# Optimization experiments

Measured on AMD Instinct MI355X. Metric: run time of the kernel, lower is better.

The kernel has to match this reference:

```python
import jax, jax.numpy as jnp
import numpy as np

D_MODEL = 1024
N_INPUT = 4096
N_PROCESS = 2048
D_ROUTING = 256
TEMPERATURE = 0.5
LN_EPS = 1e-5


def _gelu(x):
    return jax.nn.gelu(x, approximate=False)  # torch F.gelu default (erf)


def setup_inputs() -> dict:
    key = jax.random.key(0)
    ks = jax.random.split(key, 10)
    B, S = 8, 2048
    x = jax.random.normal(ks[0], (B, S, D_MODEL), dtype=jnp.float32)
    # GlobalRouter query_net: Linear(d_model, 2*d_routing) -> GELU -> LayerNorm -> Linear(2*d_routing, d_routing)
    W1 = jax.random.normal(ks[1], (2 * D_ROUTING, D_MODEL), dtype=jnp.float32) * (2.0 / (D_MODEL + 2 * D_ROUTING)) ** 0.5 * 1.414
    b1 = jnp.zeros((2 * D_ROUTING,), dtype=jnp.float32)
    ln_g = jnp.ones((2 * D_ROUTING,), dtype=jnp.float32)
    ln_b = jnp.zeros((2 * D_ROUTING,), dtype=jnp.float32)
    W2 = jax.random.normal(ks[2], (D_ROUTING, 2 * D_ROUTING), dtype=jnp.float32) * (2.0 / (3 * D_ROUTING)) ** 0.5 * 1.414
    b2 = jnp.zeros((D_ROUTING,), dtype=jnp.float32)
    neuron_keys = jax.random.normal(ks[3], (N_INPUT, D_ROUTING), dtype=jnp.float32) / D_ROUTING ** 0.5 * 1.414
    input_patterns = jax.random.normal(ks[4], (N_INPUT, D_MODEL), dtype=jnp.float32) / D_MODEL ** 0.5 * 1.414
    process_weights = jax.random.normal(ks[5], (N_PROCESS, N_INPUT), dtype=jnp.float32) / N_INPUT ** 0.5 * 1.414
    process_outputs = jax.random.normal(ks[6], (N_PROCESS, D_MODEL), dtype=jnp.float32) / D_MODEL ** 0.5 * 1.414
    return {
        'x': x, 'k_input': 2048, 'k_process': 1024,
        'W1': W1, 'b1': b1, 'ln_g': ln_g, 'ln_b': ln_b, 'W2': W2, 'b2': b2,
        'neuron_keys': neuron_keys, 'input_patterns': input_patterns,
        'process_weights': process_weights, 'process_outputs': process_outputs,
    }


def _forward(x, k_input, k_process, W1, b1, ln_g, ln_b, W2, b2,
             neuron_keys, input_patterns, process_weights, process_outputs):
    B, S, d_model = x.shape
    # ---- GlobalRouter ----
    gctx = jnp.max(x, axis=1)                                  # [B, d_model]
    h = _gelu(gctx @ W1.T + b1)                                # [B, 2*d_routing]
    mu = jnp.mean(h, axis=-1, keepdims=True)
    var = jnp.mean((h - mu) ** 2, axis=-1, keepdims=True)
    h = (h - mu) * jax.lax.rsqrt(var + LN_EPS) * ln_g + ln_b
    query = h @ W2.T + b2                                      # [B, d_routing]
    logits = (query @ neuron_keys.T) / D_ROUTING ** 0.5        # [B, n_input]
    probs = jax.nn.softmax(logits / TEMPERATURE, axis=-1)
    _, input_idx = jax.lax.top_k(logits, k_input)              # [B, k_input]
    one_hot = jnp.zeros_like(probs).at[jnp.arange(B)[:, None], input_idx].set(1.0)
    routing_weights = jax.lax.stop_gradient(one_hot - probs) + probs  # STE
    # ---- input neuron stage ----
    input_acts = _gelu(jnp.einsum('bsd,nd->bsn', x, input_patterns))   # [B,S,n_input]
    weighted = input_acts * routing_weights[:, None, :]
    sel_in = jnp.take_along_axis(weighted, input_idx[:, None, :], axis=2)  # [B,S,k_input]
    # gather process weight columns per batch: [B, n_process, k_input]
    W_sel = jnp.transpose(process_weights[:, input_idx], (1, 0, 2))
    process_acts = _gelu(jnp.einsum('bsk,bpk->bsp', sel_in, W_sel))    # [B,S,n_process]
    # ---- process neuron stage ----
    process_scores = jnp.mean(process_acts, axis=1)                    # [B,n_process]
    _, process_idx = jax.lax.top_k(process_scores, k_process)          # [B,k_process]
    sel_proc = jnp.take_along_axis(process_acts, process_idx[:, None, :], axis=2)  # [B,S,k_process]
    out_sel = process_outputs[process_idx]                             # [B,k_process,d_model]
    return jnp.einsum('bsp,bpd->bsd', sel_proc, out_sel)


def reference(x, k_input, k_process, W1, b1, ln_g, ln_b, W2, b2,
              neuron_keys, input_patterns, process_weights, process_outputs):
    return _forward(x, k_input, k_process, W1, b1, ln_g, ln_b, W2, b2,
                    neuron_keys, input_patterns, process_weights, process_outputs)
```

## Files before the change

### kernel.cpp

```cpp
#include <hip/hip_runtime.h>
#include <stdint.h>

#define B_  8
#define S_  2048
#define DM  1024
#define NI  4096
#define NP  2048
#define DR  256
#define H2  512
#define KI  2048
#define KP  1024
#define LDW 40

typedef __attribute__((ext_vector_type(8))) short bf16x8;
typedef __attribute__((ext_vector_type(4))) float f32x4;
typedef unsigned short ushort;
typedef unsigned int uint;

__device__ __forceinline__ float gelu_erf(float v){
    return 0.5f * v * (1.0f + erff(v * 0.7071067811865476f));
}
__device__ __forceinline__ ushort f2b(float f){
    union { float f; uint u; } a; a.f = f;
    uint r = a.u + 0x7fffu + ((a.u >> 16) & 1u);
    return (ushort)(r >> 16);
}
__device__ __forceinline__ float b2f(ushort u){
    union { uint u; float f; } a; a.u = ((uint)u) << 16; return a.f;
}
__device__ __forceinline__ void cvt8(const float* p, uint4& H, uint4& L){
    uint h[4], l[4];
    #pragma unroll
    for(int i = 0; i < 4; i++){
        ushort h0 = f2b(p[2*i]);   float f0 = b2f(h0); ushort l0 = f2b(p[2*i]   - f0);
        ushort h1 = f2b(p[2*i+1]); float f1 = b2f(h1); ushort l1 = f2b(p[2*i+1] - f1);
        h[i] = (uint)h0 | ((uint)h1 << 16);
        l[i] = (uint)l0 | ((uint)l1 << 16);
    }
    H = uint4{h[0],h[1],h[2],h[3]};
    L = uint4{l[0],l[1],l[2],l[3]};
}
__device__ __forceinline__ void gload_lds16(const void* g, void* l){
    __builtin_amdgcn_global_load_lds((const __attribute__((address_space(1))) void*)g,
                                     (__attribute__((address_space(3))) void*)l, 16, 0, 0);
}

__global__ __launch_bounds__(256) void k_gpart_cvt(const float* __restrict__ x,
                                                   float* __restrict__ gpart,
                                                   ushort* __restrict__ xh,
                                                   ushort* __restrict__ xl){
    int b = blockIdx.x >> 5, ch = blockIdx.x & 31;
    size_t row0 = (size_t)b*S_ + (size_t)ch*64;
    const float4* xb = (const float4*)(x + row0*DM);
    int t = threadIdx.x;
    float4 m = float4{-3.402823466e38f, -3.402823466e38f, -3.402823466e38f, -3.402823466e38f};
    for(int r = 0; r < 64; r++){
        float4 v = xb[(size_t)r*(DM/4) + t];
        ushort hx = f2b(v.x), hy = f2b(v.y), hz = f2b(v.z), hw = f2b(v.w);
        uint2 H{ (uint)hx | ((uint)hy << 16), (uint)hz | ((uint)hw << 16) };
        uint2 L{ (uint)f2b(v.x - b2f(hx)) | ((uint)f2b(v.y - b2f(hy)) << 16),
                 (uint)f2b(v.z - b2f(hz)) | ((uint)f2b(v.w - b2f(hw)) << 16) };
        ((uint2*)(xh + (row0 + r)*DM))[t] = H;
        ((uint2*)(xl + (row0 + r)*DM))[t] = L;
        m.x = fmaxf(m.x, v.x); m.y = fmaxf(m.y, v.y);
        m.z = fmaxf(m.z, v.z); m.w = fmaxf(m.w, v.w);
    }
    ((float4*)(gpart + (size_t)(b*32 + ch)*DM))[t] = m;
}

__global__ __launch_bounds__(256) void k_cvt(const float* __restrict__ src,
                                             ushort* __restrict__ hi,
                                             ushort* __restrict__ lo){
    size_t idx = (size_t)blockIdx.x*256 + threadIdx.x;
    float f[8];
    *(float4*)(f)     = ((const float4*)src)[idx*2];
    *(float4*)(f + 4) = ((const float4*)src)[idx*2 + 1];
    uint4 H, L; cvt8(f, H, L);
    ((uint4*)hi)[idx] = H;
    ((uint4*)lo)[idx] = L;
}

__global__ __launch_bounds__(256) void k_cvt1(const float* __restrict__ src,
                                              ushort* __restrict__ dst){
    size_t idx = (size_t)blockIdx.x*256 + threadIdx.x;
    float f[8];
    *(float4*)(f)     = ((const float4*)src)[idx*2];
    *(float4*)(f + 4) = ((const float4*)src)[idx*2 + 1];
    uint o[4];
    #pragma unroll
    for(int i = 0; i < 4; i++)
        o[i] = (uint)f2b(f[2*i]) | ((uint)f2b(f[2*i+1]) << 16);
    ((uint4*)dst)[idx] = uint4{o[0], o[1], o[2], o[3]};
}

__global__ __launch_bounds__(256) void k_h(const float* __restrict__ gpart,
                                           const float* __restrict__ W1,
                                           const float* __restrict__ b1,
                                           float* __restrict__ h){
    __shared__ float g[DM];
    int b = blockIdx.x >> 3, ig = blockIdx.x & 7;
    int t = threadIdx.x;
    for(int d = t; d < DM; d += 256){
        float m = gpart[(size_t)(b*32)*DM + d];
        for(int c = 1; c < 32; c++) m = fmaxf(m, gpart[(size_t)(b*32 + c)*DM + d]);
        g[d] = m;
    }
    __syncthreads();
    int i  = ig*64 + (t >> 2);
    int dq = (t & 3) * 256;
    const float* wr = W1 + (size_t)i*DM + dq;
    const float* gg = g + dq;
    float s = 0.f;
    for(int d = 0; d < 256; d++) s = fmaf(gg[d], wr[d], s);
    s += __shfl_xor(s, 1);
    s += __shfl_xor(s, 2);
    if((t & 3) == 0) h[b*H2 + i] = gelu_erf(s + b1[i]);
}

__global__ __launch_bounds__(256) void k_query(const float* __restrict__ h,
                                               const float* __restrict__ lng,
                                               const float* __restrict__ lnb,
                                               const float* __restrict__ W2,
                                               const float* __restrict__ b2,
                                               float* __restrict__ query){
    __shared__ float hn[H2];
    __shared__ float red[4];
    int b = blockIdx.x >> 2, qg = blockIdx.x & 3;
    int t = threadIdx.x;
    float v0 = h[b*H2 + t], v1 = h[b*H2 + 256 + t];
    float s = v0 + v1;
    for(int o = 32; o > 0; o >>= 1) s += __shfl_down(s, o);
    if((t & 63) == 0) red[t >> 6] = s;
    __syncthreads();
    float mean = (red[0] + red[1] + red[2] + red[3]) * (1.f/H2);
    __syncthreads();
    float d0 = v0 - mean, d1 = v1 - mean;
    float sq = d0*d0 + d1*d1;
    for(int o = 32; o > 0; o >>= 1) sq += __shfl_down(sq, o);
    if((t & 63) == 0) red[t >> 6] = sq;
    __syncthreads();
    float var  = (red[0] + red[1] + red[2] + red[3]) * (1.f/H2);
    float rstd = rsqrtf(var + 1e-5f);
    hn[t]       = d0*rstd*lng[t]       + lnb[t];
    hn[256 + t] = d1*rstd*lng[256 + t] + lnb[256 + t];
    __syncthreads();
    int q  = qg*64 + (t >> 2);
    int iq = (t & 3) * 128;
    const float* wr = W2 + (size_t)q*H2 + iq;
    float acc = 0.f;
    for(int i2 = 0; i2 < 128; i2++) acc = fmaf(hn[iq + i2], wr[i2], acc);
    acc += __shfl_xor(acc, 1);
    acc += __shfl_xor(acc, 2);
    if((t & 3) == 0) query[b*DR + q] = acc + b2[q];
}

__global__ __launch_bounds__(256) void k_logits(const float* __restrict__ query,
                                                const float* __restrict__ nk,
                                                float* __restrict__ logits){
    __shared__ float q[DR];
    int b = blockIdx.x >> 4, ng = blockIdx.x & 15;
    int t = threadIdx.x;
    if(t < DR) q[t] = query[b*DR + t];
    __syncthreads();
    int n = ng*256 + t;
    const float* kr = nk + (size_t)n*DR;
    float s = 0.f;
    for(int i = 0; i < DR; i++) s = fmaf(q[i], kr[i], s);
    logits[b*NI + n] = s * 0.0625f;
}

template<int N_, int KSEL>
__global__ __launch_bounds__(256) void k_topk(const float* __restrict__ vals,
                                              int* __restrict__ idxout){
    __shared__ unsigned u[N_];
    __shared__ int redc[4];
    __shared__ int sc[256];
    int t = threadIdx.x;
    size_t vbase = (size_t)blockIdx.x * N_;
    size_t obase = (size_t)blockIdx.x * KSEL;
    for(int i = t; i < N_; i += 256){
        unsigned bits = __float_as_uint(vals[vbase + i]);
        u[i] = (bits & 0x80000000u) ? ~bits : (bits | 0x80000000u);
    }
    __syncthreads();
    unsigned lo = 0u, hi = 0xFFFFFFFFu;
    while(lo < hi){
        unsigned mid = lo + (unsigned)((((unsigned long long)(hi - lo)) + 1ull) >> 1);
        int c = 0;
        for(int i = t; i < N_; i += 256) c += (u[i] >= mid) ? 1 : 0;
        for(int o = 32; o > 0; o >>= 1) c += __shfl_down(c, o);
        if((t & 63) == 0) redc[t >> 6] = c;
        __syncthreads();
        int tot = redc[0] + redc[1] + redc[2] + redc[3];
        if(tot >= KSEL) lo = mid; else hi = mid - 1;
        __syncthreads();
    }
    unsigned T = lo;
    const int PER = N_ / 256;
    int base = t * PER;
    int lgt = 0, leq = 0;
    for(int j = 0; j < PER; j++){
        unsigned v = u[base + j];
        lgt += (v > T) ? 1 : 0; leq += (v == T) ? 1 : 0;
    }
    sc[t] = (lgt << 16) | leq;
    __syncthreads();
    for(int o = 1; o < 256; o <<= 1){
        int add = (t >= o) ? sc[t - o] : 0;
        __syncthreads();
        sc[t] += add;
        __syncthreads();
    }
    int need = KSEL - (sc[255] >> 16);
    int ex = (t == 0) ? 0 : sc[t - 1];
    int pos = (ex >> 16) + ((ex & 0xffff) < need ? (ex & 0xffff) : need);
    int eq = ex & 0xffff;
    for(int j = 0; j < PER; j++){
        unsigned v = u[base + j];
        if(v > T){ idxout[obase + pos++] = base + j; }
        else if(v == T){ if(eq < need){ idxout[obase + pos++] = base + j; } eq++; }
    }
}

__global__ __launch_bounds__(256) void k_gemm1(const ushort* __restrict__ xh,
                                               const ushort* __restrict__ xl,
                                               const ushort* __restrict__ ph,
                                               const ushort* __restrict__ pl,
                                               const int* __restrict__ iidx,
                                               ushort* __restrict__ selh,
                                               ushort* __restrict__ sell, int b0){
    __shared__ __align__(16) ushort Ah[2][128*32], Al[2][128*32], Bh[2][128*32], Bl[2][128*32];
    __shared__ int rowmap[128];
    int t = threadIdx.x;
    int g = blockIdx.x >> 8, rest = blockIdx.x & 255;
    int b = b0 + g;
    int mb = rest >> 4, nb = rest & 15;
    int m0 = mb*128, n0 = nb*128;
    ushort* selh_g = selh + (size_t)g*S_*KI;
    ushort* sell_g = sell + (size_t)g*S_*KI;
    if(t < 128) rowmap[t] = iidx[(size_t)b*KI + n0 + t];
    __syncthreads();
    int w = t >> 6, l = t & 63;
    int lr = l >> 2, lc = l & 3;
    int r0 = 32*w + lr, r1 = r0 + 16;
    const ushort* pAh0 = xh + ((size_t)b*S_ + m0 + r0)*DM + lc*8;
    const ushort* pAh1 = xh + ((size_t)b*S_ + m0 + r1)*DM + lc*8;
    const ushort* pAl0 = xl + ((size_t)b*S_ + m0 + r0)*DM + lc*8;
    const ushort* pAl1 = xl + ((size_t)b*S_ + m0 + r1)*DM + lc*8;
    const ushort* pBh0 = ph + (size_t)rowmap[r0]*DM + lc*8;
    const ushort* pBh1 = ph + (size_t)rowmap[r1]*DM + lc*8;
    const ushort* pBl0 = pl + (size_t)rowmap[r0]*DM + lc*8;
    const ushort* pBl1 = pl + (size_t)rowmap[r1]*DM + lc*8;
    int d0 = w*1024, d1 = d0 + 512;
    #define STG1(BUF, KO) do{ \
        gload_lds16(pAh0 + (KO), &Ah[BUF][d0]); \
        gload_lds16(pAh1 + (KO), &Ah[BUF][d1]); \
        gload_lds16(pAl0 + (KO), &Al[BUF][d0]); \
        gload_lds16(pAl1 + (KO), &Al[BUF][d1]); \
        gload_lds16(pBh0 + (KO), &Bh[BUF][d0]); \
        gload_lds16(pBh1 + (KO), &Bh[BUF][d1]); \
        gload_lds16(pBl0 + (KO), &Bl[BUF][d0]); \
        gload_lds16(pBl1 + (KO), &Bl[BUF][d1]); \
    }while(0)
    STG1(0, 0);
    int lm = l & 15, q = l >> 4;
    int mbase = (w >> 1)*64, nbase = (w & 1)*64;
    f32x4 acc[4][4];
    #pragma unroll
    for(int i = 0; i < 4; i++)
      #pragma unroll
      for(int j = 0; j < 4; j++) acc[i][j] = f32x4{0.f,0.f,0.f,0.f};
    int cur = 0;
    for(int k0 = 0; k0 < DM; k0 += 32){
        if(k0 + 32 < DM){
            STG1(cur^1, k0 + 32);
            asm volatile("s_waitcnt vmcnt(8)" ::: "memory");
        }else{
            asm volatile("s_waitcnt vmcnt(0)" ::: "memory");
        }
        __builtin_amdgcn_s_barrier();
        asm volatile("" ::: "memory");
        bf16x8 ahf[4], alf[4];
        #pragma unroll
        for(int mt = 0; mt < 4; mt++){
            ahf[mt] = *(const bf16x8*)(&Ah[cur][(mbase + mt*16 + lm)*32 + q*8]);
            alf[mt] = *(const bf16x8*)(&Al[cur][(mbase + mt*16 + lm)*32 + q*8]);
        }
        __builtin_amdgcn_s_setprio(1);
        #pragma unroll
        for(int nt = 0; nt < 4; nt++){
            bf16x8 bhf = *(const bf16x8*)(&Bh[cur][(nbase + nt*16 + lm)*32 + q*8]);
            bf16x8 blf = *(const bf16x8*)(&Bl[cur][(nbase + nt*16 + lm)*32 + q*8]);
            #pragma unroll
            for(int mt = 0; mt < 4; mt++){
                acc[mt][nt] = __builtin_amdgcn_mfma_f32_16x16x32_bf16(ahf[mt], bhf, acc[mt][nt], 0, 0, 0);
                acc[mt][nt] = __builtin_amdgcn_mfma_f32_16x16x32_bf16(ahf[mt], blf, acc[mt][nt], 0, 0, 0);
                acc[mt][nt] = __builtin_amdgcn_mfma_f32_16x16x32_bf16(alf[mt], bhf, acc[mt][nt], 0, 0, 0);
            }
        }
        __builtin_amdgcn_s_setprio(0);
        asm volatile("s_waitcnt lgkmcnt(0)" ::: "memory");
        __builtin_amdgcn_s_barrier();
        asm volatile("" ::: "memory");
        cur ^= 1;
    }
    #undef STG1
    #pragma unroll
    for(int mt = 0; mt < 4; mt++)
      #pragma unroll
      for(int nt = 0; nt < 4; nt++){
        int col = n0 + nbase + nt*16 + lm;
        #pragma unroll
        for(int i = 0; i < 4; i++){
            int row = m0 + mbase + mt*16 + q*4 + i;
            float gv = gelu_erf(acc[mt][nt][i]);
            ushort hbits = f2b(gv);
            selh_g[(size_t)row*KI + col] = hbits;
            sell_g[(size_t)row*KI + col] = f2b(gv - b2f(hbits));
        }
      }
}

__global__ __launch_bounds__(256) void k_gather_wsel(const float* __restrict__ pw,
                                                     const int* __restrict__ iidx,
                                                     ushort* __restrict__ wh,
                                                     ushort* __restrict__ wl,
                                                     float* __restrict__ scores, int b0){
    int g = blockIdx.x >> 8, pc = blockIdx.x & 255;
    int b = b0 + g;
    ushort* wh_g = wh + (size_t)g*NP*KI;
    ushort* wl_g = wl + (size_t)g*NP*KI;
    int t = threadIdx.x;
    if(t < 8) scores[(size_t)b*NP + pc*8 + t] = 0.f;
    int j0 = t*8;
    int k8[8];
    *(int4*)(k8)     = *(const int4*)(iidx + (size_t)b*KI + j0);
    *(int4*)(k8 + 4) = *(const int4*)(iidx + (size_t)b*KI + j0 + 4);
    for(int r2 = 0; r2 < 8; r2++){
        int p = pc*8 + r2;
        const float* row = pw + (size_t)p*NI;
        uint hh[4], ll[4];
        #pragma unroll
        for(int i = 0; i < 4; i++){
            float v0 = row[k8[2*i]], v1 = row[k8[2*i+1]];
            ushort h0 = f2b(v0), h1 = f2b(v1);
            hh[i] = (uint)h0 | ((uint)h1 << 16);
            ll[i] = (uint)f2b(v0 - b2f(h0)) | ((uint)f2b(v1 - b2f(h1)) << 16);
        }
        *(uint4*)(wh_g + (size_t)p*KI + j0) = uint4{hh[0],hh[1],hh[2],hh[3]};
        *(uint4*)(wl_g + (size_t)p*KI + j0) = uint4{ll[0],ll[1],ll[2],ll[3]};
    }
}

__global__ __launch_bounds__(256) void k_gemm2(const ushort* __restrict__ selh,
                                               const ushort* __restrict__ sell,
                                               const ushort* __restrict__ wh,
                                               const ushort* __restrict__ wl,
                                               ushort* __restrict__ acts,
                                               float* __restrict__ scores, int b0){
    __shared__ __align__(16) ushort Ah[2][128*32], Al[2][128*32], Bh[2][128*32], Bl[2][128*32];
    __shared__ float colsum[128];
    int t = threadIdx.x;
    int g = blockIdx.x >> 8, rest = blockIdx.x & 255;
    int b = b0 + g;
    int mb = rest >> 4, nb = rest & 15;
    int m0 = mb*128, n0 = nb*128;
    const ushort* selh_g = selh + (size_t)g*S_*KI;
    const ushort* sell_g = sell + (size_t)g*S_*KI;
    const ushort* wh_g   = wh   + (size_t)g*NP*KI;
    const ushort* wl_g   = wl   + (size_t)g*NP*KI;
    ushort* acts_g = acts + (size_t)g*S_*NP;
    int w = t >> 6, l = t & 63;
    int lr = l >> 2, lc = l & 3;
    int r0 = 32*w + lr, r1 = r0 + 16;
    const ushort* pAh0 = selh_g + (size_t)(m0 + r0)*KI + lc*8;
    const ushort* pAh1 = selh_g + (size_t)(m0 + r1)*KI + lc*8;
    const ushort* pAl0 = sell_g + (size_t)(m0 + r0)*KI + lc*8;
    const ushort* pAl1 = sell_g + (size_t)(m0 + r1)*KI + lc*8;
    const ushort* pBh0 = wh_g + (size_t)(n0 + r0)*KI + lc*8;
    const ushort* pBh1 = wh_g + (size_t)(n0 + r1)*KI + lc*8;
    const ushort* pBl0 = wl_g + (size_t)(n0 + r0)*KI + lc*8;
    const ushort* pBl1 = wl_g + (size_t)(n0 + r1)*KI + lc*8;
    int d0 = w*1024, d1 = d0 + 512;
    #define STG2(BUF, KO) do{ \
        gload_lds16(pAh0 + (KO), &Ah[BUF][d0]); \
        gload_lds16(pAh1 + (KO), &Ah[BUF][d1]); \
        gload_lds16(pAl0 + (KO), &Al[BUF][d0]); \
        gload_lds16(pAl1 + (KO), &Al[BUF][d1]); \
        gload_lds16(pBh0 + (KO), &Bh[BUF][d0]); \
        gload_lds16(pBh1 + (KO), &Bh[BUF][d1]); \
        gload_lds16(pBl0 + (KO), &Bl[BUF][d0]); \
        gload_lds16(pBl1 + (KO), &Bl[BUF][d1]); \
    }while(0)
    STG2(0, 0);
    int lm = l & 15, q = l >> 4;
    int mbase = (w >> 1)*64, nbase = (w & 1)*64;
    f32x4 acc[4][4];
    #pragma unroll
    for(int i = 0; i < 4; i++)
      #pragma unroll
      for(int j = 0; j < 4; j++) acc[i][j] = f32x4{0.f,0.f,0.f,0.f};
    int cur = 0;
    for(int k0 = 0; k0 < KI; k0 += 32){
        if(k0 + 32 < KI){
            STG2(cur^1, k0 + 32);
            asm volatile("s_waitcnt vmcnt(8)" ::: "memory");
        }else{
            asm volatile("s_waitcnt vmcnt(0)" ::: "memory");
        }
        __builtin_amdgcn_s_barrier();
        asm volatile("" ::: "memory");
        bf16x8 ahf[4], alf[4];
        #pragma unroll
        for(int mt = 0; mt < 4; mt++){
            ahf[mt] = *(const bf16x8*)(&Ah[cur][(mbase + mt*16 + lm)*32 + q*8]);
            alf[mt] = *(const bf16x8*)(&Al[cur][(mbase + mt*16 + lm)*32 + q*8]);
        }
        __builtin_amdgcn_s_setprio(1);
        #pragma unroll
        for(int nt = 0; nt < 4; nt++){
            bf16x8 bhf = *(const bf16x8*)(&Bh[cur][(nbase + nt*16 + lm)*32 + q*8]);
            bf16x8 blf = *(const bf16x8*)(&Bl[cur][(nbase + nt*16 + lm)*32 + q*8]);
            #pragma unroll
            for(int mt = 0; mt < 4; mt++){
                acc[mt][nt] = __builtin_amdgcn_mfma_f32_16x16x32_bf16(ahf[mt], bhf, acc[mt][nt], 0, 0, 0);
                acc[mt][nt] = __builtin_amdgcn_mfma_f32_16x16x32_bf16(ahf[mt], blf, acc[mt][nt], 0, 0, 0);
                acc[mt][nt] = __builtin_amdgcn_mfma_f32_16x16x32_bf16(alf[mt], bhf, acc[mt][nt], 0, 0, 0);
            }
        }
        __builtin_amdgcn_s_setprio(0);
        asm volatile("s_waitcnt lgkmcnt(0)" ::: "memory");
        __builtin_amdgcn_s_barrier();
        asm volatile("" ::: "memory");
        cur ^= 1;
    }
    #undef STG2
    if(t < 128) colsum[t] = 0.f;
    __syncthreads();
    #pragma unroll
    for(int mt = 0; mt < 4; mt++)
      #pragma unroll
      for(int nt = 0; nt < 4; nt++){
        int cb = nbase + nt*16 + lm;
        float s4 = 0.f;
        #pragma unroll
        for(int i = 0; i < 4; i++){
            int row = m0 + mbase + mt*16 + q*4 + i;
            float gv = gelu_erf(acc[mt][nt][i]);
            s4 += gv;
            acts_g[(size_t)row*NP + n0 + cb] = f2b(gv);
        }
        atomicAdd(&colsum[cb], s4);
      }
    __syncthreads();
    if(t < 128) atomicAdd(&scores[(size_t)b*NP + n0 + t], colsum[t]);
}

__global__ __launch_bounds__(256) void k_gather_selacts(const ushort* __restrict__ acts,
                                                        const int* __restrict__ pidx,
                                                        ushort* __restrict__ selacts, int b0){
    int g = blockIdx.x >> 6, sc_ = blockIdx.x & 63;
    int b = b0 + g;
    const ushort* acts_g = acts + (size_t)g*S_*NP;
    ushort* selacts_g = selacts + (size_t)g*S_*KP;
    int t = threadIdx.x;
    int j0 = t*4;
    int4 p4 = *(const int4*)(pidx + (size_t)b*KP + j0);
    const ushort* Ab = acts_g    + ((size_t)sc_*32)*NP;
    ushort*       Ob = selacts_g + ((size_t)sc_*32)*KP;
    for(int r2 = 0; r2 < 32; r2++){
        const ushort* Ar = Ab + (size_t)r2*NP;
        ushort o0 = Ar[p4.x], o1 = Ar[p4.y], o2 = Ar[p4.z], o3 = Ar[p4.w];
        uint2 ov{ (uint)o0 | ((uint)o1 << 16), (uint)o2 | ((uint)o3 << 16) };
        *(uint2*)(Ob + (size_t)r2*KP + j0) = ov;
    }
}

__global__ __launch_bounds__(256) void k_gemm3(const ushort* __restrict__ selacts,
                                               const ushort* __restrict__ poutb,
                                               const int* __restrict__ pidx,
                                               float* __restrict__ out, int b0){
    __shared__ __align__(16) ushort As[2][128*32];
    __shared__ __align__(16) ushort Bs[2][128*LDW];
    __shared__ int pix[KP];
    int t = threadIdx.x;
    int g = blockIdx.x >> 7, rest = blockIdx.x & 127;
    int b = b0 + g;
    int mb = rest >> 3, nb = rest & 7;
    int m0 = mb*128, n0 = nb*128;
    const ushort* sel_g = selacts + (size_t)g*S_*KP;
    int w = t >> 6, l = t & 63;
    int lr = l >> 2, lc = l & 3;
    int r0 = 32*w + lr, r1 = r0 + 16;
    const ushort* pA0 = sel_g + (size_t)(m0 + r0)*KP + lc*8;
    const ushort* pA1 = sel_g + (size_t)(m0 + r1)*KP + lc*8;
    int d0 = w*1024, d1 = d0 + 512;
    gload_lds16(pA0, &As[0][d0]);
    gload_lds16(pA1, &As[0][d1]);
    for(int i = t; i < KP; i += 256) pix[i] = pidx[(size_t)b*KP + i];
    __syncthreads();
    int kk = t >> 3, nc = (t & 7)*16;
    uint4 B0, B1;
    {
        const ushort* bg = poutb + (size_t)pix[kk]*DM + n0 + nc;
        B0 = *(const uint4*)(bg); B1 = *(const uint4*)(bg + 8);
    }
    int lm = l & 15, q = l >> 4;
    int mbase = (w >> 1)*64, nbase = (w & 1)*64;
    f32x4 acc[4][4];
    #pragma unroll
    for(int i = 0; i < 4; i++)
      #pragma unroll
      for(int j = 0; j < 4; j++) acc[i][j] = f32x4{0.f,0.f,0.f,0.f};
    for(int k0 = 0; k0 < KP; k0 += 32){
        int cur = (k0 >> 5) & 1;
        {
            const ushort* pb0 = (const ushort*)&B0;
            const ushort* pb1 = (const ushort*)&B1;
            #pragma unroll
            for(int c = 0; c < 8; c++) Bs[cur][(nc + c)*LDW + kk]     = pb0[c];
            #pragma unroll
            for(int c = 0; c < 8; c++) Bs[cur][(nc + 8 + c)*LDW + kk] = pb1[c];
        }
        if(k0 + 32 < KP){
            gload_lds16(pA0 + (k0 + 32), &As[cur^1][d0]);
            gload_lds16(pA1 + (k0 + 32), &As[cur^1][d1]);
            asm volatile("s_waitcnt vmcnt(2)" ::: "memory");
        }else{
            asm volatile("s_waitcnt vmcnt(0)" ::: "memory");
        }
        asm volatile("s_waitcnt lgkmcnt(0)" ::: "memory");
        __builtin_amdgcn_s_barrier();
        asm volatile("" ::: "memory");
        if(k0 + 32 < KP){
            const ushort* bg = poutb + (size_t)pix[k0 + 32 + kk]*DM + n0 + nc;
            B0 = *(const uint4*)(bg); B1 = *(const uint4*)(bg + 8);
        }
        bf16x8 af[4];
        #pragma unroll
        for(int mt = 0; mt < 4; mt++)
            af[mt] = *(const bf16x8*)(&As[cur][(mbase + mt*16 + lm)*32 + q*8]);
        __builtin_amdgcn_s_setprio(1);
        #pragma unroll
        for(int nt = 0; nt < 4; nt++){
            bf16x8 bf = *(const bf16x8*)(&Bs[cur][(nbase + nt*16 + lm)*LDW + q*8]);
            #pragma unroll
            for(int mt = 0; mt < 4; mt++)
                acc[mt][nt] = __builtin_amdgcn_mfma_f32_16x16x32_bf16(af[mt], bf, acc[mt][nt], 0, 0, 0);
        }
        __builtin_amdgcn_s_setprio(0);
        asm volatile("s_waitcnt lgkmcnt(0)" ::: "memory");
        __builtin_amdgcn_s_barrier();
        asm volatile("" ::: "memory");
    }
    float* Cb = out + (size_t)b*S_*DM;
    #pragma unroll
    for(int mt = 0; mt < 4; mt++)
      #pragma unroll
      for(int nt = 0; nt < 4; nt++){
        int col = n0 + nbase + nt*16 + lm;
        #pragma unroll
        for(int i = 0; i < 4; i++){
            int row = m0 + mbase + mt*16 + q*4 + i;
            Cb[(size_t)row*DM + col] = acc[mt][nt][i];
        }
      }
}

extern "C" void kernel_launch(void* const* d_in, const int* in_sizes, int n_in,
                              void* d_out, int out_size, void* d_ws, size_t ws_size,
                              hipStream_t stream){
    const float* x    = (const float*)d_in[0];
    const float* W1   = (const float*)d_in[3];
    const float* b1   = (const float*)d_in[4];
    const float* lng  = (const float*)d_in[5];
    const float* lnb  = (const float*)d_in[6];
    const float* W2   = (const float*)d_in[7];
    const float* b2   = (const float*)d_in[8];
    const float* nk   = (const float*)d_in[9];
    const float* patt = (const float*)d_in[10];
    const float* pw   = (const float*)d_in[11];
    const float* pout = (const float*)d_in[12];
    float* out = (float*)d_out;

    auto al256 = [](size_t v){ return (v + 255) & ~(size_t)255; };
    const size_t fixed =
        al256((size_t)B_*32*DM*4) + al256((size_t)B_*H2*4) + al256((size_t)B_*DR*4) +
        al256((size_t)B_*NI*4)    + al256((size_t)B_*KI*4) + al256((size_t)B_*NP*4) +
        al256((size_t)B_*KP*4) +
        2*al256((size_t)B_*S_*DM*2) + 2*al256((size_t)NI*DM*2) + al256((size_t)NP*DM*2);
    const size_t perb = (size_t)S_*KI*2*2 + (size_t)NP*KI*2*2 + (size_t)S_*NP*2 + (size_t)S_*KP*2 + 6*256;
    int G = 8;
    while(G > 1 && fixed + (size_t)G*perb > ws_size) G >>= 1;
    if(fixed + (size_t)G*perb > ws_size) return;

    char* wsp = (char*)d_ws;
    size_t off = 0;
    auto alloc = [&](size_t bytes) -> void* {
        void* p = wsp + off;
        off += (bytes + 255) & ~(size_t)255;
        return p;
    };
    float*  gpart   = (float*) alloc((size_t)B_*32*DM*4);
    float*  h       = (float*) alloc((size_t)B_*H2*4);
    float*  query   = (float*) alloc((size_t)B_*DR*4);
    float*  logits  = (float*) alloc((size_t)B_*NI*4);
    int*    iidx    = (int*)   alloc((size_t)B_*KI*4);
    float*  scores  = (float*) alloc((size_t)B_*NP*4);
    int*    pidx    = (int*)   alloc((size_t)B_*KP*4);
    ushort* xh      = (ushort*)alloc((size_t)B_*S_*DM*2);
    ushort* xl      = (ushort*)alloc((size_t)B_*S_*DM*2);
    ushort* patth   = (ushort*)alloc((size_t)NI*DM*2);
    ushort* pattl   = (ushort*)alloc((size_t)NI*DM*2);
    ushort* poutb   = (ushort*)alloc((size_t)NP*DM*2);
    ushort* selh    = (ushort*)alloc((size_t)G*S_*KI*2);
    ushort* sell    = (ushort*)alloc((size_t)G*S_*KI*2);
    ushort* wselh   = (ushort*)alloc((size_t)G*NP*KI*2);
    ushort* wsell   = (ushort*)alloc((size_t)G*NP*KI*2);
    ushort* acts    = (ushort*)alloc((size_t)G*S_*NP*2);
    ushort* selacts = (ushort*)alloc((size_t)G*S_*KP*2);

    dim3 blk(256);
    k_gpart_cvt<<<B_*32, blk, 0, stream>>>(x, gpart, xh, xl);
    k_cvt   <<<(NI*DM/8)/256, blk, 0, stream>>>(patt, patth, pattl);
    k_cvt1  <<<(NP*DM/8)/256, blk, 0, stream>>>(pout, poutb);
    k_h     <<<64,  blk, 0, stream>>>(gpart, W1, b1, h);
    k_query <<<32,  blk, 0, stream>>>(h, lng, lnb, W2, b2, query);
    k_logits<<<128, blk, 0, stream>>>(query, nk, logits);
    k_topk<NI, KI><<<B_, blk, 0, stream>>>(logits, iidx);
    for(int b0 = 0; b0 < B_; b0 += G){
        k_gemm1        <<<G*256, blk, 0, stream>>>(xh, xl, patth, pattl, iidx, selh, sell, b0);
        k_gather_wsel  <<<G*256, blk, 0, stream>>>(pw, iidx, wselh, wsell, scores, b0);
        k_gemm2        <<<G*256, blk, 0, stream>>>(selh, sell, wselh, wsell, acts, scores, b0);
        k_topk<NP, KP> <<<G,     blk, 0, stream>>>(scores + (size_t)b0*NP, pidx + (size_t)b0*KP);
        k_gather_selacts<<<G*64, blk, 0, stream>>>(acts, pidx, selacts, b0);
        k_gemm3        <<<G*128, blk, 0, stream>>>(selacts, poutb, pidx, out, b0);
    }
}
```

Measured before the change: 1.297 ms.

## Fuse preprocessing kernels, merge gather into GEMM1 launch, widen topk and logits

```diff
diff --git a/kernel.cpp b/kernel.cpp
--- a/kernel.cpp
+++ b/kernel.cpp
@@ -45,52 +45,53 @@
                                      (__attribute__((address_space(3))) void*)l, 16, 0, 0);
 }
 
-__global__ __launch_bounds__(256) void k_gpart_cvt(const float* __restrict__ x,
-                                                   float* __restrict__ gpart,
-                                                   ushort* __restrict__ xh,
-                                                   ushort* __restrict__ xl){
-    int b = blockIdx.x >> 5, ch = blockIdx.x & 31;
-    size_t row0 = (size_t)b*S_ + (size_t)ch*64;
-    const float4* xb = (const float4*)(x + row0*DM);
-    int t = threadIdx.x;
-    float4 m = float4{-3.402823466e38f, -3.402823466e38f, -3.402823466e38f, -3.402823466e38f};
-    for(int r = 0; r < 64; r++){
-        float4 v = xb[(size_t)r*(DM/4) + t];
-        ushort hx = f2b(v.x), hy = f2b(v.y), hz = f2b(v.z), hw = f2b(v.w);
-        uint2 H{ (uint)hx | ((uint)hy << 16), (uint)hz | ((uint)hw << 16) };
-        uint2 L{ (uint)f2b(v.x - b2f(hx)) | ((uint)f2b(v.y - b2f(hy)) << 16),
-                 (uint)f2b(v.z - b2f(hz)) | ((uint)f2b(v.w - b2f(hw)) << 16) };
-        ((uint2*)(xh + (row0 + r)*DM))[t] = H;
-        ((uint2*)(xl + (row0 + r)*DM))[t] = L;
-        m.x = fmaxf(m.x, v.x); m.y = fmaxf(m.y, v.y);
-        m.z = fmaxf(m.z, v.z); m.w = fmaxf(m.w, v.w);
-    }
-    ((float4*)(gpart + (size_t)(b*32 + ch)*DM))[t] = m;
-}
-
-__global__ __launch_bounds__(256) void k_cvt(const float* __restrict__ src,
-                                             ushort* __restrict__ hi,
-                                             ushort* __restrict__ lo){
-    size_t idx = (size_t)blockIdx.x*256 + threadIdx.x;
-    float f[8];
-    *(float4*)(f)     = ((const float4*)src)[idx*2];
-    *(float4*)(f + 4) = ((const float4*)src)[idx*2 + 1];
-    uint4 H, L; cvt8(f, H, L);
-    ((uint4*)hi)[idx] = H;
-    ((uint4*)lo)[idx] = L;
-}
-
-__global__ __launch_bounds__(256) void k_cvt1(const float* __restrict__ src,
-                                              ushort* __restrict__ dst){
-    size_t idx = (size_t)blockIdx.x*256 + threadIdx.x;
-    float f[8];
-    *(float4*)(f)     = ((const float4*)src)[idx*2];
-    *(float4*)(f + 4) = ((const float4*)src)[idx*2 + 1];
-    uint o[4];
-    #pragma unroll
-    for(int i = 0; i < 4; i++)
-        o[i] = (uint)f2b(f[2*i]) | ((uint)f2b(f[2*i+1]) << 16);
-    ((uint4*)dst)[idx] = uint4{o[0], o[1], o[2], o[3]};
+__global__ __launch_bounds__(256) void k_pre(const float* __restrict__ x,
+                                             const float* __restrict__ patt,
+                                             const float* __restrict__ pout,
+                                             float* __restrict__ gpart,
+                                             ushort* __restrict__ xh,
+                                             ushort* __restrict__ xl,
+                                             ushort* __restrict__ patth,
+                                             ushort* __restrict__ pattl,
+                                             ushort* __restrict__ poutb){
+    int bid = blockIdx.x;
+    int t = threadIdx.x;
+    if(bid < 512){
+        int b = bid >> 6, ch = bid & 63;
+        size_t row0 = (size_t)b*S_ + (size_t)ch*32;
+        const float4* xb = (const float4*)(x + row0*DM);
+        float4 m = float4{-3.402823466e38f, -3.402823466e38f, -3.402823466e38f, -3.402823466e38f};
+        for(int r = 0; r < 32; r++){
+            float4 v = xb[(size_t)r*(DM/4) + t];
+            ushort hx = f2b(v.x), hy = f2b(v.y), hz = f2b(v.z), hw = f2b(v.w);
+            uint2 H{ (uint)hx | ((uint)hy << 16), (uint)hz | ((uint)hw << 16) };
+            uint2 L{ (uint)f2b(v.x - b2f(hx)) | ((uint)f2b(v.y - b2f(hy)) << 16),
+                     (uint)f2b(v.z - b2f(hz)) | ((uint)f2b(v.w - b2f(hw)) << 16) };
+            ((uint2*)(xh + (row0 + r)*DM))[t] = H;
+            ((uint2*)(xl + (row0 + r)*DM))[t] = L;
+            m.x = fmaxf(m.x, v.x); m.y = fmaxf(m.y, v.y);
+            m.z = fmaxf(m.z, v.z); m.w = fmaxf(m.w, v.w);
+        }
+        ((float4*)(gpart + (size_t)(b*64 + ch)*DM))[t] = m;
+    }else if(bid < 2560){
+        size_t idx = (size_t)(bid - 512)*256 + t;
+        float f[8];
+        *(float4*)(f)     = ((const float4*)patt)[idx*2];
+        *(float4*)(f + 4) = ((const float4*)patt)[idx*2 + 1];
+        uint4 H, L; cvt8(f, H, L);
+        ((uint4*)patth)[idx] = H;
+        ((uint4*)pattl)[idx] = L;
+    }else{
+        size_t idx = (size_t)(bid - 2560)*256 + t;
+        float f[8];
+        *(float4*)(f)     = ((const float4*)pout)[idx*2];
+        *(float4*)(f + 4) = ((const float4*)pout)[idx*2 + 1];
+        uint o[4];
+        #pragma unroll
+        for(int i = 0; i < 4; i++)
+            o[i] = (uint)f2b(f[2*i]) | ((uint)f2b(f[2*i+1]) << 16);
+        ((uint4*)poutb)[idx] = uint4{o[0], o[1], o[2], o[3]};
+    }
 }
 
 __global__ __launch_bounds__(256) void k_h(const float* __restrict__ gpart,
@@ -101,8 +102,8 @@
     int b = blockIdx.x >> 3, ig = blockIdx.x & 7;
     int t = threadIdx.x;
     for(int d = t; d < DM; d += 256){
-        float m = gpart[(size_t)(b*32)*DM + d];
-        for(int c = 1; c < 32; c++) m = fmaxf(m, gpart[(size_t)(b*32 + c)*DM + d]);
+        float m = gpart[(size_t)(b*64)*DM + d];
+        for(int c = 1; c < 64; c++) m = fmaxf(m, gpart[(size_t)(b*64 + c)*DM + d]);
         g[d] = m;
     }
     __syncthreads();
@@ -157,28 +158,35 @@
 __global__ __launch_bounds__(256) void k_logits(const float* __restrict__ query,
                                                 const float* __restrict__ nk,
                                                 float* __restrict__ logits){
-    __shared__ float q[DR];
+    __shared__ float4 q4[DR/4];
     int b = blockIdx.x >> 4, ng = blockIdx.x & 15;
     int t = threadIdx.x;
-    if(t < DR) q[t] = query[b*DR + t];
-    __syncthreads();
-    int n = ng*256 + t;
-    const float* kr = nk + (size_t)n*DR;
-    float s = 0.f;
-    for(int i = 0; i < DR; i++) s = fmaf(q[i], kr[i], s);
-    logits[b*NI + n] = s * 0.0625f;
+    if(t < 64) q4[t] = ((const float4*)(query + (size_t)b*DR))[t];
+    __syncthreads();
+    int w = t >> 6, lane = t & 63;
+    float4 qv = q4[lane];
+    int nbase = ng*256 + w*64;
+    #pragma unroll 2
+    for(int i = 0; i < 64; i++){
+        int n = nbase + i;
+        float4 v = ((const float4*)(nk + (size_t)n*DR))[lane];
+        float p = v.x*qv.x + v.y*qv.y + v.z*qv.z + v.w*qv.w;
+        p += __shfl_down(p, 32); p += __shfl_down(p, 16); p += __shfl_down(p, 8);
+        p += __shfl_down(p, 4);  p += __shfl_down(p, 2);  p += __shfl_down(p, 1);
+        if(lane == 0) logits[(size_t)b*NI + n] = p * 0.0625f;
+    }
 }
 
 template<int N_, int KSEL>
-__global__ __launch_bounds__(256) void k_topk(const float* __restrict__ vals,
-                                              int* __restrict__ idxout){
+__global__ __launch_bounds__(1024) void k_topk(const float* __restrict__ vals,
+                                               int* __restrict__ idxout){
     __shared__ unsigned u[N_];
-    __shared__ int redc[4];
-    __shared__ int sc[256];
+    __shared__ int redc[16];
+    __shared__ int sc[1024];
     int t = threadIdx.x;
     size_t vbase = (size_t)blockIdx.x * N_;
     size_t obase = (size_t)blockIdx.x * KSEL;
-    for(int i = t; i < N_; i += 256){
+    for(int i = t; i < N_; i += 1024){
         unsigned bits = __float_as_uint(vals[vbase + i]);
         u[i] = (bits & 0x80000000u) ? ~bits : (bits | 0x80000000u);
     }
@@ -187,16 +195,18 @@
     while(lo < hi){
         unsigned mid = lo + (unsigned)((((unsigned long long)(hi - lo)) + 1ull) >> 1);
         int c = 0;
-        for(int i = t; i < N_; i += 256) c += (u[i] >= mid) ? 1 : 0;
+        for(int i = t; i < N_; i += 1024) c += (u[i] >= mid) ? 1 : 0;
         for(int o = 32; o > 0; o >>= 1) c += __shfl_down(c, o);
         if((t & 63) == 0) redc[t >> 6] = c;
         __syncthreads();
-        int tot = redc[0] + redc[1] + redc[2] + redc[3];
+        int tot = 0;
+        #pragma unroll
+        for(int i = 0; i < 16; i++) tot += redc[i];
         if(tot >= KSEL) lo = mid; else hi = mid - 1;
         __syncthreads();
     }
     unsigned T = lo;
-    const int PER = N_ / 256;
+    const int PER = N_ / 1024;
     int base = t * PER;
     int lgt = 0, leq = 0;
     for(int j = 0; j < PER; j++){
@@ -205,13 +215,13 @@
     }
     sc[t] = (lgt << 16) | leq;
     __syncthreads();
-    for(int o = 1; o < 256; o <<= 1){
+    for(int o = 1; o < 1024; o <<= 1){
         int add = (t >= o) ? sc[t - o] : 0;
         __syncthreads();
         sc[t] += add;
         __syncthreads();
     }
-    int need = KSEL - (sc[255] >> 16);
+    int need = KSEL - (sc[1023] >> 16);
     int ex = (t == 0) ? 0 : sc[t - 1];
     int pos = (ex >> 16) + ((ex & 0xffff) < need ? (ex & 0xffff) : need);
     int eq = ex & 0xffff;
@@ -222,18 +232,62 @@
     }
 }
 
-__global__ __launch_bounds__(256) void k_gemm1(const ushort* __restrict__ xh,
-                                               const ushort* __restrict__ xl,
-                                               const ushort* __restrict__ ph,
-                                               const ushort* __restrict__ pl,
-                                               const int* __restrict__ iidx,
-                                               ushort* __restrict__ selh,
-                                               ushort* __restrict__ sell, int b0){
-    __shared__ __align__(16) ushort Ah[2][128*32], Al[2][128*32], Bh[2][128*32], Bl[2][128*32];
-    __shared__ int rowmap[128];
-    int t = threadIdx.x;
-    int g = blockIdx.x >> 8, rest = blockIdx.x & 255;
+__global__ __launch_bounds__(256) void k_stage1(const ushort* __restrict__ xh,
+                                                const ushort* __restrict__ xl,
+                                                const ushort* __restrict__ ph,
+                                                const ushort* __restrict__ pl,
+                                                const float* __restrict__ pw,
+                                                const int* __restrict__ iidx,
+                                                ushort* __restrict__ selh,
+                                                ushort* __restrict__ sell,
+                                                ushort* __restrict__ wh,
+                                                ushort* __restrict__ wl,
+                                                float* __restrict__ scores, int b0){
+    __shared__ __align__(16) ushort sm[33024];
+    int t = threadIdx.x;
+    int role = blockIdx.x & 1;
+    int id   = blockIdx.x >> 1;
+    int g = id >> 8;
     int b = b0 + g;
+    if(role == 1){
+        float* row = (float*)sm;
+        int pc = id & 255;
+        ushort* wh_g = wh + (size_t)g*NP*KI;
+        ushort* wl_g = wl + (size_t)g*NP*KI;
+        if(t < 8) scores[(size_t)b*NP + pc*8 + t] = 0.f;
+        int j0 = t*8;
+        int k8[8];
+        *(int4*)(k8)     = *(const int4*)(iidx + (size_t)b*KI + j0);
+        *(int4*)(k8 + 4) = *(const int4*)(iidx + (size_t)b*KI + j0 + 4);
+        for(int r2 = 0; r2 < 8; r2++){
+            int p = pc*8 + r2;
+            const float4* src = (const float4*)(pw + (size_t)p*NI);
+            float4 rv0 = src[t], rv1 = src[t + 256], rv2 = src[t + 512], rv3 = src[t + 768];
+            __syncthreads();
+            ((float4*)row)[t]       = rv0;
+            ((float4*)row)[t + 256] = rv1;
+            ((float4*)row)[t + 512] = rv2;
+            ((float4*)row)[t + 768] = rv3;
+            __syncthreads();
+            uint hh[4], ll[4];
+            #pragma unroll
+            for(int i = 0; i < 4; i++){
+                float v0 = row[k8[2*i]], v1 = row[k8[2*i+1]];
+                ushort h0 = f2b(v0), h1 = f2b(v1);
+                hh[i] = (uint)h0 | ((uint)h1 << 16);
+                ll[i] = (uint)f2b(v0 - b2f(h0)) | ((uint)f2b(v1 - b2f(h1)) << 16);
+            }
+            *(uint4*)(wh_g + (size_t)p*KI + j0) = uint4{hh[0],hh[1],hh[2],hh[3]};
+            *(uint4*)(wl_g + (size_t)p*KI + j0) = uint4{ll[0],ll[1],ll[2],ll[3]};
+        }
+        return;
+    }
+    ushort* Ah = sm;
+    ushort* Al = sm + 8192;
+    ushort* Bh = sm + 16384;
+    ushort* Bl = sm + 24576;
+    int* rowmap = (int*)(sm + 32768);
+    int rest = id & 255;
     int mb = rest >> 4, nb = rest & 15;
     int m0 = mb*128, n0 = nb*128;
     ushort* selh_g = selh + (size_t)g*S_*KI;
@@ -253,14 +307,14 @@
     const ushort* pBl1 = pl + (size_t)rowmap[r1]*DM + lc*8;
     int d0 = w*1024, d1 = d0 + 512;
     #define STG1(BUF, KO) do{ \
-        gload_lds16(pAh0 + (KO), &Ah[BUF][d0]); \
-        gload_lds16(pAh1 + (KO), &Ah[BUF][d1]); \
-        gload_lds16(pAl0 + (KO), &Al[BUF][d0]); \
-        gload_lds16(pAl1 + (KO), &Al[BUF][d1]); \
-        gload_lds16(pBh0 + (KO), &Bh[BUF][d0]); \
-        gload_lds16(pBh1 + (KO), &Bh[BUF][d1]); \
-        gload_lds16(pBl0 + (KO), &Bl[BUF][d0]); \
-        gload_lds16(pBl1 + (KO), &Bl[BUF][d1]); \
+        gload_lds16(pAh0 + (KO), &Ah[(BUF)*4096 + d0]); \
+        gload_lds16(pAh1 + (KO), &Ah[(BUF)*4096 + d1]); \
+        gload_lds16(pAl0 + (KO), &Al[(BUF)*4096 + d0]); \
+        gload_lds16(pAl1 + (KO), &Al[(BUF)*4096 + d1]); \
+        gload_lds16(pBh0 + (KO), &Bh[(BUF)*4096 + d0]); \
+        gload_lds16(pBh1 + (KO), &Bh[(BUF)*4096 + d1]); \
+        gload_lds16(pBl0 + (KO), &Bl[(BUF)*4096 + d0]); \
+        gload_lds16(pBl1 + (KO), &Bl[(BUF)*4096 + d1]); \
     }while(0)
     STG1(0, 0);
     int lm = l & 15, q = l >> 4;
@@ -283,14 +337,14 @@
         bf16x8 ahf[4], alf[4];
         #pragma unroll
         for(int mt = 0; mt < 4; mt++){
-            ahf[mt] = *(const bf16x8*)(&Ah[cur][(mbase + mt*16 + lm)*32 + q*8]);
-            alf[mt] = *(const bf16x8*)(&Al[cur][(mbase + mt*16 + lm)*32 + q*8]);
+            ahf[mt] = *(const bf16x8*)(&Ah[cur*4096 + (mbase + mt*16 + lm)*32 + q*8]);
+            alf[mt] = *(const bf16x8*)(&Al[cur*4096 + (mbase + mt*16 + lm)*32 + q*8]);
         }
         __builtin_amdgcn_s_setprio(1);
         #pragma unroll
         for(int nt = 0; nt < 4; nt++){
-            bf16x8 bhf = *(const bf16x8*)(&Bh[cur][(nbase + nt*16 + lm)*32 + q*8]);
-            bf16x8 blf = *(const bf16x8*)(&Bl[cur][(nbase + nt*16 + lm)*32 + q*8]);
+            bf16x8 bhf = *(const bf16x8*)(&Bh[cur*4096 + (nbase + nt*16 + lm)*32 + q*8]);
+            bf16x8 blf = *(const bf16x8*)(&Bl[cur*4096 + (nbase + nt*16 + lm)*32 + q*8]);
             #pragma unroll
             for(int mt = 0; mt < 4; mt++){
                 acc[mt][nt] = __builtin_amdgcn_mfma_f32_16x16x32_bf16(ahf[mt], bhf, acc[mt][nt], 0, 0, 0);
@@ -319,37 +373,6 @@
             sell_g[(size_t)row*KI + col] = f2b(gv - b2f(hbits));
         }
       }
-}
-
-__global__ __launch_bounds__(256) void k_gather_wsel(const float* __restrict__ pw,
-                                                     const int* __restrict__ iidx,
-                                                     ushort* __restrict__ wh,
-                                                     ushort* __restrict__ wl,
-                                                     float* __restrict__ scores, int b0){
-    int g = blockIdx.x >> 8, pc = blockIdx.x & 255;
-    int b = b0 + g;
-    ushort* wh_g = wh + (size_t)g*NP*KI;
-    ushort* wl_g = wl + (size_t)g*NP*KI;
-    int t = threadIdx.x;
-    if(t < 8) scores[(size_t)b*NP + pc*8 + t] = 0.f;
-    int j0 = t*8;
-    int k8[8];
-    *(int4*)(k8)     = *(const int4*)(iidx + (size_t)b*KI + j0);
-    *(int4*)(k8 + 4) = *(const int4*)(iidx + (size_t)b*KI + j0 + 4);
-    for(int r2 = 0; r2 < 8; r2++){
-        int p = pc*8 + r2;
-        const float* row = pw + (size_t)p*NI;
-        uint hh[4], ll[4];
-        #pragma unroll
-        for(int i = 0; i < 4; i++){
-            float v0 = row[k8[2*i]], v1 = row[k8[2*i+1]];
-            ushort h0 = f2b(v0), h1 = f2b(v1);
-            hh[i] = (uint)h0 | ((uint)h1 << 16);
-            ll[i] = (uint)f2b(v0 - b2f(h0)) | ((uint)f2b(v1 - b2f(h1)) << 16);
-        }
-        *(uint4*)(wh_g + (size_t)p*KI + j0) = uint4{hh[0],hh[1],hh[2],hh[3]};
-        *(uint4*)(wl_g + (size_t)p*KI + j0) = uint4{ll[0],ll[1],ll[2],ll[3]};
-    }
 }
 
 __global__ __launch_bounds__(256) void k_gemm2(const ushort* __restrict__ selh,
@@ -585,7 +608,7 @@
 
     auto al256 = [](size_t v){ return (v + 255) & ~(size_t)255; };
     const size_t fixed =
-        al256((size_t)B_*32*DM*4) + al256((size_t)B_*H2*4) + al256((size_t)B_*DR*4) +
+        al256((size_t)B_*64*DM*4) + al256((size_t)B_*H2*4) + al256((size_t)B_*DR*4) +
         al256((size_t)B_*NI*4)    + al256((size_t)B_*KI*4) + al256((size_t)B_*NP*4) +
         al256((size_t)B_*KP*4) +
         2*al256((size_t)B_*S_*DM*2) + 2*al256((size_t)NI*DM*2) + al256((size_t)NP*DM*2);
@@ -601,7 +624,7 @@
         off += (bytes + 255) & ~(size_t)255;
         return p;
     };
-    float*  gpart   = (float*) alloc((size_t)B_*32*DM*4);
+    float*  gpart   = (float*) alloc((size_t)B_*64*DM*4);
     float*  h       = (float*) alloc((size_t)B_*H2*4);
     float*  query   = (float*) alloc((size_t)B_*DR*4);
     float*  logits  = (float*) alloc((size_t)B_*NI*4);
@@ -621,18 +644,16 @@
     ushort* selacts = (ushort*)alloc((size_t)G*S_*KP*2);
 
     dim3 blk(256);
-    k_gpart_cvt<<<B_*32, blk, 0, stream>>>(x, gpart, xh, xl);
-    k_cvt   <<<(NI*DM/8)/256, blk, 0, stream>>>(patt, patth, pattl);
-    k_cvt1  <<<(NP*DM/8)/256, blk, 0, stream>>>(pout, poutb);
+    k_pre   <<<3584, blk, 0, stream>>>(x, patt, pout, gpart, xh, xl, patth, pattl, poutb);
     k_h     <<<64,  blk, 0, stream>>>(gpart, W1, b1, h);
     k_query <<<32,  blk, 0, stream>>>(h, lng, lnb, W2, b2, query);
     k_logits<<<128, blk, 0, stream>>>(query, nk, logits);
-    k_topk<NI, KI><<<B_, blk, 0, stream>>>(logits, iidx);
+    k_topk<NI, KI><<<B_, dim3(1024), 0, stream>>>(logits, iidx);
     for(int b0 = 0; b0 < B_; b0 += G){
-        k_gemm1        <<<G*256, blk, 0, stream>>>(xh, xl, patth, pattl, iidx, selh, sell, b0);
-        k_gather_wsel  <<<G*256, blk, 0, stream>>>(pw, iidx, wselh, wsell, scores, b0);
+        k_stage1       <<<G*512, blk, 0, stream>>>(xh, xl, patth, pattl, pw, iidx,
+                                                   selh, sell, wselh, wsell, scores, b0);
         k_gemm2        <<<G*256, blk, 0, stream>>>(selh, sell, wselh, wsell, acts, scores, b0);
-        k_topk<NP, KP> <<<G,     blk, 0, stream>>>(scores + (size_t)b0*NP, pidx + (size_t)b0*KP);
+        k_topk<NP, KP> <<<G,     dim3(1024), 0, stream>>>(scores + (size_t)b0*NP, pidx + (size_t)b0*KP);
         k_gather_selacts<<<G*64, blk, 0, stream>>>(acts, pidx, selacts, b0);
         k_gemm3        <<<G*128, blk, 0, stream>>>(selacts, poutb, pidx, out, b0);
     }
```

New measurement: 1.478 ms. 13.9% more time.
